# Kernel tuning notes

Measured on AMD Instinct MI355X. Metric: run time of the kernel, lower is better.

The kernel has to match this reference:

```python
import jax, jax.numpy as jnp
import numpy as np

PATCH = 7            # args.corr_size (local correlation window)
R = PATCH // 2       # displacement radius


def _disps():
    return [(dy, dx) for dy in range(PATCH) for dx in range(PATCH)]


def setup_inputs() -> dict:
    key = jax.random.key(0)
    k1, k2, k3 = jax.random.split(key, 3)
    B, De, Do, T, H, W = 4, 64, 64, 4, 128, 128
    m_in = jax.random.normal(k1, (B, De, T, H, W), jnp.float32)
    m_out = jax.random.normal(k2, (B, Do, T, H, W), jnp.float32)
    q_in = jax.random.normal(k3, (B, De, H, W), jnp.float32)
    const = jnp.zeros((1,), jnp.float32)  # learnable constant (init 0)
    return {"m_in": m_in, "m_out": m_out, "q_in": q_in, "const": const}


def reference(m_in, m_out, q_in, const):
    B, De, T, H, W = m_in.shape
    Do = m_out.shape[1]
    P2 = PATCH * PATCH
    # --- functionCorrelation over all T frames at once ---
    # p[b, d, t, h, w] = sum_c q[b,c,h,w] * m_in[b,c,t,h+dy-R,w+dx-R]  (zero-padded)
    mp = jnp.pad(m_in, ((0, 0), (0, 0), (0, 0), (R, R), (R, R)))
    p = jnp.stack(
        [jnp.einsum('bchw,bcthw->bthw', q_in, mp[:, :, :, dy:dy + H, dx:dx + W])
         for dy, dx in _disps()],
        axis=1)  # [B, P2, T, H, W]  (matches torch stack(dim=2) then disp at dim=1)
    # --- softmax over stacked (P2*T [+1 const]) channels ---
    logits = p.reshape(B, P2 * T, H, W)
    cst = jnp.broadcast_to(const.reshape(1, 1, 1, 1), (B, 1, H, W))
    logits = jnp.concatenate([logits, cst], axis=1)
    attn = jax.nn.softmax(logits, axis=1)[:, :-1]  # drop constant channel
    attn = attn.reshape(B, P2, T, H, W)
    # --- functionCorrelationTranspose summed over T (attention read) ---
    # mem[b,c,h,w] = sum_{t,d} attn[b,d,t,h,w] * m_out[b,c,t,h+dy-R,w+dx-R]
    vp = jnp.pad(m_out, ((0, 0), (0, 0), (0, 0), (R, R), (R, R)))
    mem = jnp.zeros((B, Do, H, W), m_out.dtype)
    for d, (dy, dx) in enumerate(_disps()):
        mem = mem + jnp.einsum('bthw,bcthw->bchw', attn[:, d], vp[:, :, :, dy:dy + H, dx:dx + W])
    return mem, attn
```

## Files before the change

### kernel.cpp

```cpp
#include <hip/hip_runtime.h>

#define ATTN_OFF 4194304
#define WS_F4_COUNT 3407872ull

__global__ __launch_bounds__(256, 2) void k1_corr(
    const float* __restrict__ m_in, const float* __restrict__ q_in,
    float* __restrict__ out)
{
  const int p = blockIdx.x + (blockIdx.y << 2) + (blockIdx.z << 6);
  const int l = ((p & 7) << 7) + (p >> 3);
  const int bx = l & 3, by = (l >> 2) & 15, bz = l >> 6;

  const int b = bz >> 2, t = bz & 3;
  const int h0 = by * 8, w0 = bx * 32;
  const int tid = threadIdx.x;
  const int tx = tid & 31, ty = tid >> 5;
  const int h = h0 + ty, w = w0 + tx;

  __shared__ float m_s[14][42][4];
  float* const lds = &m_s[0][0][0];

  float acc[49];
#pragma unroll
  for (int d = 0; d < 49; ++d) acc[d] = 0.f;

  int goff0, goff1, goff2, loff0, loff1, loff2;
  float msk0, msk1, msk2;
  {
    const int i0 = tid;
    const int y0 = i0 / 38, x0 = i0 - 38 * y0;
    const int gy0 = h0 - 3 + y0, gx0 = w0 - 3 + x0;
    msk0 = (((unsigned)gy0 < 128u) && ((unsigned)gx0 < 128u)) ? 1.f : 0.f;
    const int gyc0 = gy0 < 0 ? 0 : (gy0 > 127 ? 127 : gy0);
    const int gxc0 = gx0 < 0 ? 0 : (gx0 > 127 ? 127 : gx0);
    goff0 = (gyc0 << 7) + gxc0;
    loff0 = (y0 * 42 + x0 + 1) << 2;

    const int i1 = tid + 256;
    const int y1 = i1 / 38, x1 = i1 - 38 * y1;
    const int gy1 = h0 - 3 + y1, gx1 = w0 - 3 + x1;
    msk1 = (((unsigned)gy1 < 128u) && ((unsigned)gx1 < 128u)) ? 1.f : 0.f;
    const int gyc1 = gy1 < 0 ? 0 : (gy1 > 127 ? 127 : gy1);
    const int gxc1 = gx1 < 0 ? 0 : (gx1 > 127 ? 127 : gx1);
    goff1 = (gyc1 << 7) + gxc1;
    loff1 = (y1 * 42 + x1 + 1) << 2;

    const int i2 = tid + 512;
    const int i2c = i2 < 532 ? i2 : 531;
    const int y2 = i2c / 38, x2 = i2c - 38 * y2;
    const int gy2 = h0 - 3 + y2, gx2 = w0 - 3 + x2;
    msk2 = (((unsigned)gy2 < 128u) && ((unsigned)gx2 < 128u)) ? 1.f : 0.f;
    const int gyc2 = gy2 < 0 ? 0 : (gy2 > 127 ? 127 : gy2);
    const int gxc2 = gx2 < 0 ? 0 : (gx2 > 127 ? 127 : gx2);
    goff2 = (gyc2 << 7) + gxc2;
    loff2 = (y2 * 42 + x2 + 1) << 2;
  }
  const bool has2 = (tid < 20);

  float4 r0, r1, r2;
  {
    const float* base = m_in + ((b * 256 + t) << 14);
    const float* p0 = base + goff0;
    r0.x = p0[0]; r0.y = p0[65536]; r0.z = p0[131072]; r0.w = p0[196608];
    const float* p1 = base + goff1;
    r1.x = p1[0]; r1.y = p1[65536]; r1.z = p1[131072]; r1.w = p1[196608];
    r2 = make_float4(0.f, 0.f, 0.f, 0.f);
    if (has2) {
      const float* p2 = base + goff2;
      r2.x = p2[0]; r2.y = p2[65536]; r2.z = p2[131072]; r2.w = p2[196608];
    }
  }

#pragma unroll 1
  for (int cc = 0; cc < 16; ++cc) {
    __syncthreads();
    *(float4*)(lds + loff0) = make_float4(r0.x*msk0, r0.y*msk0, r0.z*msk0, r0.w*msk0);
    *(float4*)(lds + loff1) = make_float4(r1.x*msk1, r1.y*msk1, r1.z*msk1, r1.w*msk1);
    if (has2)
      *(float4*)(lds + loff2) = make_float4(r2.x*msk2, r2.y*msk2, r2.z*msk2, r2.w*msk2);
    __syncthreads();

    if (cc < 15) {
      const float* base = m_in + (((b * 64 + (cc + 1) * 4) * 4 + t) << 14);
      const float* p0 = base + goff0;
      r0.x = p0[0]; r0.y = p0[65536]; r0.z = p0[131072]; r0.w = p0[196608];
      const float* p1 = base + goff1;
      r1.x = p1[0]; r1.y = p1[65536]; r1.z = p1[131072]; r1.w = p1[196608];
      if (has2) {
        const float* p2 = base + goff2;
        r2.x = p2[0]; r2.y = p2[65536]; r2.z = p2[131072]; r2.w = p2[196608];
      }
    }

    float q0[4];
#pragma unroll
    for (int k = 0; k < 4; ++k)
      q0[k] = q_in[((b * 64 + cc * 4 + k) << 14) + (h << 7) + w];
#pragma unroll
    for (int dy = 0; dy < 7; ++dy)
#pragma unroll
      for (int dx = 0; dx < 7; ++dx) {
        const float4 mv = *(const float4*)&m_s[ty + dy][tx + 1 + dx][0];
        acc[dy * 7 + dx] += q0[0]*mv.x + q0[1]*mv.y + q0[2]*mv.z + q0[3]*mv.w;
      }
  }

  const int obase = ATTN_OFF + ((b * 196 + t) << 14) + (h << 7) + w;
#pragma unroll
  for (int d = 0; d < 49; ++d)
    out[obase + ((d * 4) << 14)] = acc[d];
}

__global__ __launch_bounds__(256) void k2_softmax(
    float* __restrict__ out, const float* __restrict__ cst,
    float4* __restrict__ ws)
{
  const int tid = threadIdx.x;
  const int pl = tid & 63;
  const int t  = tid >> 6;
  const int pix = blockIdx.x * 64 + pl;
  const int b = pix >> 14, hw = pix & 16383;
  float* base = out + ATTN_OFF + ((b * 196 + t) << 14) + hw;

  float v[49];
#pragma unroll
  for (int d = 0; d < 49; ++d) v[d] = base[(d * 4) << 14];

  float mx = -1e30f;
#pragma unroll
  for (int d = 0; d < 49; ++d) mx = fmaxf(mx, v[d]);

  __shared__ float red[4][64];
  red[t][pl] = mx;
  __syncthreads();
  float M = fmaxf(fmaxf(red[0][pl], red[1][pl]), fmaxf(red[2][pl], red[3][pl]));
  M = fmaxf(M, cst[0]);
  __syncthreads();

  float s = 0.f;
#pragma unroll
  for (int d = 0; d < 49; ++d) { v[d] = __expf(v[d] - M); s += v[d]; }
  red[t][pl] = s;
  __syncthreads();
  const float l = red[0][pl] + red[1][pl] + red[2][pl] + red[3][pl]
                + __expf(cst[0] - M);
  const float inv = 1.f / l;
#pragma unroll
  for (int d = 0; d < 49; ++d) {
    const float r = v[d] * inv;
    base[(d * 4) << 14] = r;
    v[d] = r;
  }

  if (ws) {
    const int h = hw >> 7, wc = hw & 127;
    const int G    = ((h >> 1) << 2) + (wc >> 5);
    const int lane = ((h & 1) << 5) + (wc & 31);
    float4* dst = ws + (size_t)(((b * 256 + G) * 4 + t) * 13) * 64 + lane;
#pragma unroll
    for (int g = 0; g < 13; ++g) {
      float4 p;
      p.x = v[g * 4];
      p.y = (g < 12) ? v[g * 4 + 1] : 0.f;
      p.z = (g < 12) ? v[g * 4 + 2] : 0.f;
      p.w = (g < 12) ? v[g * 4 + 3] : 0.f;
      dst[g * 64] = p;
    }
  }
}

__global__ __launch_bounds__(256) void k3_read_ws(
    const float* __restrict__ m_out, float* __restrict__ out,
    const float4* __restrict__ ws)
{
  const int b = blockIdx.z >> 3, cq = blockIdx.z & 7;
  const int h0 = blockIdx.y * 8, w0 = blockIdx.x * 32;
  const int tid = threadIdx.x;
  const int tx = tid & 31, ty = tid >> 5;
  const int h = h0 + ty, w = w0 + tx;
  const int waveid = tid >> 6, lane = tid & 63;
  const int G = ((h0 >> 1) + waveid) * 4 + blockIdx.x;

  __shared__ float m_s[2][14][42][4];

  float acc[8];
#pragma unroll
  for (int i = 0; i < 8; ++i) acc[i] = 0.f;

#pragma unroll 1
  for (int t = 0; t < 4; ++t) {
    const float4* ap = ws + (size_t)(((b * 256 + G) * 4 + t) * 13) * 64 + lane;

    __syncthreads();
    {
      const float* base = m_out + (((b * 64 + cq * 8) * 4 + t) << 14);
#pragma unroll
      for (int k = 0; k < 5; ++k) {
        const int item = tid + (k << 8);
        if (item < 1064) {
          const int quad = item >= 532;
          const int rem  = item - 532 * quad;
          const int y  = rem / 38;
          const int xi = rem - 38 * y;
          const int gy = h0 - 3 + y, gx = w0 - 3 + xi;
          float4 v = make_float4(0.f, 0.f, 0.f, 0.f);
          if ((unsigned)gy < 128u && (unsigned)gx < 128u) {
            const float* p = base + (quad << 18) + (gy << 7) + gx;
            v.x = p[0];
            v.y = p[1 << 16];
            v.z = p[2 << 16];
            v.w = p[3 << 16];
          }
          *(float4*)&m_s[quad][y][xi + 1][0] = v;
        }
      }
    }
    __syncthreads();

    float4 cur = ap[0];
#pragma unroll
    for (int g = 0; g < 13; ++g) {
      float4 nxt = cur;
      if (g < 12) nxt = ap[(g + 1) * 64];
#pragma unroll
      for (int j = 0; j < 4; ++j) {
        const int d = g * 4 + j;
        if (d >= 49) break;
        const int dy = d / 7, dx = d % 7;
        const float av = (j == 0) ? cur.x : (j == 1) ? cur.y
                       : (j == 2) ? cur.z : cur.w;
#pragma unroll
        for (int q = 0; q < 2; ++q) {
          const float4 mv = *(const float4*)&m_s[q][ty + dy][tx + dx + 1][0];
          acc[q * 4 + 0] += av * mv.x;
          acc[q * 4 + 1] += av * mv.y;
          acc[q * 4 + 2] += av * mv.z;
          acc[q * 4 + 3] += av * mv.w;
        }
      }
      cur = nxt;
    }
  }

#pragma unroll
  for (int q = 0; q < 2; ++q)
#pragma unroll
    for (int k = 0; k < 4; ++k)
      out[((b * 64 + cq * 8 + q * 4 + k) << 14) + (h << 7) + w] = acc[q * 4 + k];
}

__global__ __launch_bounds__(256) void k3_read_fb(
    const float* __restrict__ m_out, float* __restrict__ out)
{
  const int b = blockIdx.z >> 2, cq = blockIdx.z & 3;
  const int h0 = blockIdx.y * 8, w0 = blockIdx.x * 32;
  const int tid = threadIdx.x;
  const int tx = tid & 31, ty = tid >> 5;
  const int h = h0 + ty, w = w0 + tx;

  __shared__ float m_s[4][14][38][4];
  const float* __restrict__ attn = out + ATTN_OFF;

  float acc[16];
#pragma unroll
  for (int i = 0; i < 16; ++i) acc[i] = 0.f;

#pragma unroll 1
  for (int t = 0; t < 4; ++t) {
    float a[49];
#pragma unroll
    for (int d = 0; d < 49; ++d)
      a[d] = attn[((b * 196 + d * 4 + t) << 14) + (h << 7) + w];

    __syncthreads();
    for (int e = tid; e < 8512; e += 256) {
      int c16 = e / 532; int rem = e - c16 * 532;
      int y = rem / 38;  int x = rem - y * 38;
      int gy = h0 - 3 + y, gx = w0 - 3 + x;
      float v = 0.f;
      if (gy >= 0 && gy < 128 && gx >= 0 && gx < 128)
        v = m_out[(((b * 64 + cq * 16 + c16) * 4 + t) << 14) + (gy << 7) + gx];
      m_s[c16 >> 2][y][x][c16 & 3] = v;
    }
    __syncthreads();

#pragma unroll
    for (int dy = 0; dy < 7; ++dy)
#pragma unroll
      for (int dx = 0; dx < 7; ++dx) {
        const float av = a[dy * 7 + dx];
#pragma unroll
        for (int q = 0; q < 4; ++q) {
          const float4 mv = *(const float4*)&m_s[q][ty + dy][tx + dx][0];
          acc[q * 4 + 0] += av * mv.x;
          acc[q * 4 + 1] += av * mv.y;
          acc[q * 4 + 2] += av * mv.z;
          acc[q * 4 + 3] += av * mv.w;
        }
      }
  }

#pragma unroll
  for (int q = 0; q < 4; ++q)
#pragma unroll
    for (int k = 0; k < 4; ++k)
      out[((b * 64 + cq * 16 + q * 4 + k) << 14) + (h << 7) + w] = acc[q * 4 + k];
}

extern "C" void kernel_launch(void* const* d_in, const int* in_sizes, int n_in,
                              void* d_out, int out_size, void* d_ws, size_t ws_size,
                              hipStream_t stream) {
  const float* m_in  = (const float*)d_in[0];
  const float* m_out = (const float*)d_in[1];
  const float* q_in  = (const float*)d_in[2];
  const float* cst   = (const float*)d_in[3];
  float* out = (float*)d_out;

  const bool use_ws = (ws_size >= WS_F4_COUNT * 16ull) && d_ws != nullptr;
  float4* ws = use_ws ? (float4*)d_ws : nullptr;

  k1_corr<<<dim3(4, 16, 16), dim3(256), 0, stream>>>(m_in, q_in, out);
  k2_softmax<<<dim3(1024), dim3(256), 0, stream>>>(out, cst, ws);
  if (use_ws)
    k3_read_ws<<<dim3(4, 16, 32), dim3(256), 0, stream>>>(m_out, out, ws);
  else
    k3_read_fb<<<dim3(4, 16, 16), dim3(256), 0, stream>>>(m_out, out);
}
```

Before: 142.2 us.

## Prefetch next frame's m_out tile into registers and remap k3 block order

```diff
diff --git a/kernel.cpp b/kernel.cpp
--- a/kernel.cpp
+++ b/kernel.cpp
@@ -173,49 +173,80 @@
     const float* __restrict__ m_out, float* __restrict__ out,
     const float4* __restrict__ ws)
 {
-  const int b = blockIdx.z >> 3, cq = blockIdx.z & 7;
-  const int h0 = blockIdx.y * 8, w0 = blockIdx.x * 32;
+  const int p = blockIdx.x + (blockIdx.y << 2) + (blockIdx.z << 6);
+  const int l = ((p & 7) << 8) + (p >> 3);
+  const int cq = l & 7;
+  const int tile = l >> 3;
+  const int bx = tile & 3, by = (tile >> 2) & 15, b = tile >> 6;
+
+  const int h0 = by * 8, w0 = bx * 32;
   const int tid = threadIdx.x;
   const int tx = tid & 31, ty = tid >> 5;
   const int h = h0 + ty, w = w0 + tx;
   const int waveid = tid >> 6, lane = tid & 63;
-  const int G = ((h0 >> 1) + waveid) * 4 + blockIdx.x;
+  const int G = ((h0 >> 1) + waveid) * 4 + bx;
 
   __shared__ float m_s[2][14][42][4];
+  float* const lds = &m_s[0][0][0][0];
 
   float acc[8];
 #pragma unroll
   for (int i = 0; i < 8; ++i) acc[i] = 0.f;
+
+  int goff0, goff1, goff2, goff3, goff4;
+  int loff0, loff1, loff2, loff3, loff4;
+  float msk0, msk1, msk2, msk3, msk4;
+#define K3_DECOMP(K, GO, LO, MS)                                           \
+  {                                                                        \
+    const int it  = (tid + (K << 8)) < 1064 ? (tid + (K << 8)) : 1063;     \
+    const int qd  = it >= 532;                                             \
+    const int rem = it - 532 * qd;                                         \
+    const int yy  = rem / 38;                                              \
+    const int xx  = rem - 38 * yy;                                         \
+    const int gy  = h0 - 3 + yy, gx = w0 - 3 + xx;                         \
+    MS = (((unsigned)gy < 128u) && ((unsigned)gx < 128u)) ? 1.f : 0.f;     \
+    const int gyc = gy < 0 ? 0 : (gy > 127 ? 127 : gy);                    \
+    const int gxc = gx < 0 ? 0 : (gx > 127 ? 127 : gx);                    \
+    GO = (qd << 18) + (gyc << 7) + gxc;                                    \
+    LO = (((qd * 14 + yy) * 42) + xx + 1) << 2;                            \
+  }
+  K3_DECOMP(0, goff0, loff0, msk0)
+  K3_DECOMP(1, goff1, loff1, msk1)
+  K3_DECOMP(2, goff2, loff2, msk2)
+  K3_DECOMP(3, goff3, loff3, msk3)
+  K3_DECOMP(4, goff4, loff4, msk4)
+#undef K3_DECOMP
+  const bool has4 = (tid < 40);
+
+  float4 r0, r1, r2, r3, r4;
+#define K3_LOAD(T)                                                         \
+  {                                                                        \
+    const float* base = m_out + (((b * 64 + cq * 8) * 4 + (T)) << 14);     \
+    const float* q;                                                        \
+    q = base + goff0; r0.x = q[0]; r0.y = q[65536]; r0.z = q[131072]; r0.w = q[196608]; \
+    q = base + goff1; r1.x = q[0]; r1.y = q[65536]; r1.z = q[131072]; r1.w = q[196608]; \
+    q = base + goff2; r2.x = q[0]; r2.y = q[65536]; r2.z = q[131072]; r2.w = q[196608]; \
+    q = base + goff3; r3.x = q[0]; r3.y = q[65536]; r3.z = q[131072]; r3.w = q[196608]; \
+    if (has4) { q = base + goff4;                                          \
+      r4.x = q[0]; r4.y = q[65536]; r4.z = q[131072]; r4.w = q[196608]; }  \
+  }
+  r4 = make_float4(0.f, 0.f, 0.f, 0.f);
+  K3_LOAD(0)
 
 #pragma unroll 1
   for (int t = 0; t < 4; ++t) {
     const float4* ap = ws + (size_t)(((b * 256 + G) * 4 + t) * 13) * 64 + lane;
 
     __syncthreads();
-    {
-      const float* base = m_out + (((b * 64 + cq * 8) * 4 + t) << 14);
-#pragma unroll
-      for (int k = 0; k < 5; ++k) {
-        const int item = tid + (k << 8);
-        if (item < 1064) {
-          const int quad = item >= 532;
-          const int rem  = item - 532 * quad;
-          const int y  = rem / 38;
-          const int xi = rem - 38 * y;
-          const int gy = h0 - 3 + y, gx = w0 - 3 + xi;
-          float4 v = make_float4(0.f, 0.f, 0.f, 0.f);
-          if ((unsigned)gy < 128u && (unsigned)gx < 128u) {
-            const float* p = base + (quad << 18) + (gy << 7) + gx;
-            v.x = p[0];
-            v.y = p[1 << 16];
-            v.z = p[2 << 16];
-            v.w = p[3 << 16];
-          }
-          *(float4*)&m_s[quad][y][xi + 1][0] = v;
-        }
-      }
-    }
-    __syncthreads();
+    *(float4*)(lds + loff0) = make_float4(r0.x*msk0, r0.y*msk0, r0.z*msk0, r0.w*msk0);
+    *(float4*)(lds + loff1) = make_float4(r1.x*msk1, r1.y*msk1, r1.z*msk1, r1.w*msk1);
+    *(float4*)(lds + loff2) = make_float4(r2.x*msk2, r2.y*msk2, r2.z*msk2, r2.w*msk2);
+    *(float4*)(lds + loff3) = make_float4(r3.x*msk3, r3.y*msk3, r3.z*msk3, r3.w*msk3);
+    if (has4)
+      *(float4*)(lds + loff4) = make_float4(r4.x*msk4, r4.y*msk4, r4.z*msk4, r4.w*msk4);
+    __syncthreads();
+
+    if (t < 3) K3_LOAD(t + 1)
 
     float4 cur = ap[0];
 #pragma unroll
@@ -241,6 +272,7 @@
       cur = nxt;
     }
   }
+#undef K3_LOAD
 
 #pragma unroll
   for (int q = 0; q < 2; ++q)
```

Measured after the change: 130.6 us. -8.2%, faster.
